# Performance work log

Measured on AMD Instinct MI355X. Metric: run time of the kernel, lower is better.

Reference implementation:

```python
import jax, jax.numpy as jnp
import numpy as np

NUM_HOP = 3
VOCAB = 32000
D = 512          # embed_dim
MEM = 60         # memory_size (> story_size -> T_A slice branch)
BS = 64
STORY = 50
SENT = 32        # max_sent_size
QLEN = 16


def positional_encoding(J, d):
    # pe[i-1, k-1] = 1 - i/J - (k/d) * (1 - 2*i/J), i in 1..J, k in 1..d
    i = jnp.arange(1, J + 1, dtype=jnp.float32)[:, None]
    k = jnp.arange(1, d + 1, dtype=jnp.float32)[None, :]
    return 1.0 - i / J - (k / d) * (1.0 - 2.0 * i / J)


def setup_inputs() -> dict:
    key = jax.random.key(0)
    kA, kT, kC, kQ = jax.random.split(key, 4)
    # stacked embedding tables A[0..num_hop], each (VOCAB, D), N(0, 0.1)
    A = jax.random.normal(kA, (NUM_HOP + 1, VOCAB, D), dtype=jnp.float32) * 0.1
    T_A = jax.random.normal(kT, (1, MEM, D), dtype=jnp.float32) * 0.1
    context = jax.random.randint(kC, (BS, STORY, SENT), 0, VOCAB)
    query = jax.random.randint(kQ, (BS, QLEN), 0, VOCAB)
    return {"context": context, "query": query, "A": A, "T_A": T_A}


def reference(context, query, A, T_A):
    # padding_idx=0: row 0 of every table is zero
    A = A.at[:, 0, :].set(0.0)
    pe = positional_encoding(SENT, D)              # (SENT, D)

    # query encoding: u = B(query).sum(axis=1), B = A[0]; dropout is identity at eval
    u = A[0][query].sum(axis=1)                    # (BS, D)

    for h in range(NUM_HOP):
        # memory embedding with positional encoding, summed over words
        m = (A[h][context] * pe).sum(axis=2)       # (BS, STORY, D)
        # temporal encoding: memory_size > story_size branch
        m = m + T_A[:, :STORY, :]
        # output embedding (no positional encoding applied in original)
        c = A[h + 1][context].sum(axis=2)          # (BS, STORY, D)
        p = jax.nn.softmax(jnp.einsum('bsd,bd->bs', m, u), axis=1)
        u = u + jnp.einsum('bs,bsd->bd', p, c)

    # W = A[-1].weight.T -> logits = u @ W
    logits = u @ A[NUM_HOP].T                      # (BS, VOCAB)
    return jax.nn.softmax(logits, axis=-1)
```

## Files before the change

kernel.cpp:

```cpp
#include <hip/hip_runtime.h>
#include <math.h>

#define NUM_HOP 3
#define VOCAB   32000
#define DIM     512
#define MEM     60
#define BS      64
#define STORY   50
#define SENT    32
#define QLEN    16

#define SZ      ((size_t)BS * STORY * DIM)
#define TBL     ((size_t)VOCAB * DIM)

typedef short v8s __attribute__((ext_vector_type(8)));
typedef float v4f __attribute__((ext_vector_type(4)));

static __device__ __forceinline__ ushort f2bf(float x) {
    union { float f; unsigned u; } v; v.f = x;
    unsigned r = (v.u + 0x7FFFu + ((v.u >> 16) & 1u)) >> 16;
    return (ushort)r;
}

__global__ __launch_bounds__(128) void k_gather(const float* __restrict__ A,
                                                const int*   __restrict__ ctx,
                                                const int*   __restrict__ query,
                                                float*       __restrict__ mw,
                                                float*       __restrict__ c,
                                                float*       __restrict__ u) {
    const unsigned blk = blockIdx.x;
    const int d = threadIdx.x * 4;
    if (blk >= 4u * BS * STORY) {
        const int b = blk - 4u * BS * STORY;
        const int* q = query + b * QLEN;
        float4 acc = make_float4(0.f, 0.f, 0.f, 0.f);
        for (int t = 0; t < QLEN; ++t) {
            const int idx = q[t];
            if (idx != 0) {
                const float4 a = *(const float4*)(A + (size_t)idx * DIM + d);
                acc.x += a.x; acc.y += a.y; acc.z += a.z; acc.w += a.w;
            }
        }
        *(float4*)(u + (size_t)b * DIM + d) = acc;
        return;
    }
    const unsigned pass = blk / (BS * STORY);
    const unsigned bs   = blk - pass * (BS * STORY);
    const float* table = A + (size_t)pass * TBL;
    const int*   cw    = ctx + bs * SENT;

    float4 m  = make_float4(0.f, 0.f, 0.f, 0.f);
    float4 cc = make_float4(0.f, 0.f, 0.f, 0.f);
    const float invD = 1.0f / (float)DIM;
    #pragma unroll 8
    for (int w = 0; w < SENT; ++w) {
        const int idx = cw[w];
        if (idx == 0) continue;
        const float4 a = *(const float4*)(table + (size_t)idx * DIM + d);
        const float aw = 1.0f - (float)(w + 1) * (1.0f / (float)SENT);
        const float bw = 1.0f - (float)(2 * (w + 1)) * (1.0f / (float)SENT);
        m.x = fmaf(a.x, aw - bw * (float)(d + 1) * invD, m.x);
        m.y = fmaf(a.y, aw - bw * (float)(d + 2) * invD, m.y);
        m.z = fmaf(a.z, aw - bw * (float)(d + 3) * invD, m.z);
        m.w = fmaf(a.w, aw - bw * (float)(d + 4) * invD, m.w);
        cc.x += a.x; cc.y += a.y; cc.z += a.z; cc.w += a.w;
    }
    if (pass < 3) *(float4*)(mw + (size_t)pass * SZ + (size_t)bs * DIM + d) = m;
    if (pass > 0) *(float4*)(c + (size_t)(pass - 1) * SZ + (size_t)bs * DIM + d) = cc;
}

__global__ __launch_bounds__(512) void k_hops(const float* __restrict__ mw,
                                              const float* __restrict__ c,
                                              const float* __restrict__ T_A,
                                              const float* __restrict__ u_g,
                                              ushort*      __restrict__ ubf) {
    const int b    = blockIdx.x;
    const int tid  = threadIdx.x;
    const int wave = tid >> 6;
    const int lane = tid & 63;
    __shared__ float su[DIM];
    __shared__ float sw[64];
    __shared__ float up[8][DIM];

    su[tid] = u_g[(size_t)b * DIM + tid];
    __syncthreads();

    for (int h = 0; h < NUM_HOP; ++h) {
        const float* mwh = mw + (size_t)h * SZ + (size_t)b * STORY * DIM;
        const float* ch  = c  + (size_t)h * SZ + (size_t)b * STORY * DIM;

        const float4 u0 = *(const float4*)(&su[lane * 8]);
        const float4 u1 = *(const float4*)(&su[lane * 8 + 4]);
        for (int s = wave; s < STORY; s += 8) {
            const float* mrow = mwh + (size_t)s * DIM + lane * 8;
            const float* trow = T_A + (size_t)s * DIM + lane * 8;
            const float4 m0 = *(const float4*)(mrow);
            const float4 m1 = *(const float4*)(mrow + 4);
            const float4 t0 = *(const float4*)(trow);
            const float4 t1 = *(const float4*)(trow + 4);
            float p = (m0.x + t0.x) * u0.x + (m0.y + t0.y) * u0.y +
                      (m0.z + t0.z) * u0.z + (m0.w + t0.w) * u0.w +
                      (m1.x + t1.x) * u1.x + (m1.y + t1.y) * u1.y +
                      (m1.z + t1.z) * u1.z + (m1.w + t1.w) * u1.w;
            for (int off = 32; off; off >>= 1) p += __shfl_down(p, off);
            if (lane == 0) sw[s] = p;
        }
        __syncthreads();

        if (tid < 64) {
            const float v = (tid < STORY) ? sw[tid] : -1e30f;
            float mx = v;
            for (int off = 32; off; off >>= 1) mx = fmaxf(mx, __shfl_down(mx, off));
            mx = __shfl(mx, 0);
            const float e = (tid < STORY) ? __expf(v - mx) : 0.f;
            float sm = e;
            for (int off = 32; off; off >>= 1) sm += __shfl_down(sm, off);
            sm = __shfl(sm, 0);
            if (tid < STORY) sw[tid] = e / sm;
        }
        __syncthreads();

        float4 a0 = make_float4(0.f, 0.f, 0.f, 0.f);
        float4 a1 = make_float4(0.f, 0.f, 0.f, 0.f);
        for (int s = wave; s < STORY; s += 8) {
            const float  w    = sw[s];
            const float* crow = ch + (size_t)s * DIM + lane * 8;
            const float4 c0 = *(const float4*)(crow);
            const float4 c1 = *(const float4*)(crow + 4);
            a0.x = fmaf(w, c0.x, a0.x); a0.y = fmaf(w, c0.y, a0.y);
            a0.z = fmaf(w, c0.z, a0.z); a0.w = fmaf(w, c0.w, a0.w);
            a1.x = fmaf(w, c1.x, a1.x); a1.y = fmaf(w, c1.y, a1.y);
            a1.z = fmaf(w, c1.z, a1.z); a1.w = fmaf(w, c1.w, a1.w);
        }
        *(float4*)(&up[wave][lane * 8])     = a0;
        *(float4*)(&up[wave][lane * 8 + 4]) = a1;
        __syncthreads();

        float add = 0.f;
        #pragma unroll
        for (int w = 0; w < 8; ++w) add += up[w][tid];
        su[tid] += add;
        __syncthreads();
    }

    ubf[(size_t)b * DIM + tid] = f2bf(su[tid]);
}

__global__ __launch_bounds__(256) void k_logits(const float*  __restrict__ A3,
                                                const ushort* __restrict__ ubf,
                                                float*        __restrict__ out) {
    __shared__ ushort Abf[64 * 128];
    __shared__ ushort Ubf[64 * 128];
    const int tid  = threadIdx.x;
    const int lane = tid & 63;
    const int wave = tid >> 6;
    const int i16  = lane & 15;
    const int quad = lane >> 4;
    const int row0 = blockIdx.x * 64;

    v4f acc[4];
    #pragma unroll
    for (int nt = 0; nt < 4; ++nt) acc[nt] = (v4f){0.f, 0.f, 0.f, 0.f};

    for (int ko = 0; ko < 4; ++ko) {
        __syncthreads();
        #pragma unroll
        for (int it = 0; it < 4; ++it) {
            const int i = it * 256 + tid;
            const int r = i >> 4, g = i & 15;
            const float* src = A3 + ((size_t)(row0 + r)) * DIM + ko * 128 + g * 8;
            const float4 f0 = *(const float4*)(src);
            const float4 f1 = *(const float4*)(src + 4);
            union { ushort h[8]; uint4 q; } pk;
            pk.h[0] = f2bf(f0.x); pk.h[1] = f2bf(f0.y);
            pk.h[2] = f2bf(f0.z); pk.h[3] = f2bf(f0.w);
            pk.h[4] = f2bf(f1.x); pk.h[5] = f2bf(f1.y);
            pk.h[6] = f2bf(f1.z); pk.h[7] = f2bf(f1.w);
            *(uint4*)(&Abf[r * 128 + ((g ^ (r & 7)) * 8)]) = pk.q;
        }
        #pragma unroll
        for (int it = 0; it < 4; ++it) {
            const int i = it * 256 + tid;
            const int n = i >> 4, g = i & 15;
            const uint4 v = *(const uint4*)(ubf + (size_t)n * DIM + ko * 128 + g * 8);
            *(uint4*)(&Ubf[n * 128 + ((g ^ (n & 7)) * 8)]) = v;
        }
        __syncthreads();

        const int arow = wave * 16 + i16;
        #pragma unroll
        for (int ki = 0; ki < 4; ++ki) {
            const int ga = ki * 4 + quad;
            const v8s a = *(const v8s*)(&Abf[arow * 128 + ((ga ^ (arow & 7)) * 8)]);
            #pragma unroll
            for (int nt = 0; nt < 4; ++nt) {
                const int n = nt * 16 + i16;
                const v8s bb = *(const v8s*)(&Ubf[n * 128 + ((ga ^ (n & 7)) * 8)]);
                acc[nt] = __builtin_amdgcn_mfma_f32_16x16x32_bf16(a, bb, acc[nt], 0, 0, 0);
            }
        }
    }

    const int vbase = row0 + wave * 16 + quad * 4;
    #pragma unroll
    for (int nt = 0; nt < 4; ++nt) {
        const int bcol = nt * 16 + i16;
        #pragma unroll
        for (int r = 0; r < 4; ++r)
            out[(size_t)bcol * VOCAB + vbase + r] = acc[nt][r];
    }
}

__global__ __launch_bounds__(1024) void k_vsm(float* __restrict__ out) {
    const int b   = blockIdx.x;
    const int tid = threadIdx.x;
    float* row = out + (size_t)b * VOCAB;
    __shared__ float red[16];
    __shared__ float bc;

    float x[32];
    #pragma unroll
    for (int k = 0; k < 31; ++k) x[k] = row[tid + k * 1024];
    const bool extra = (tid < VOCAB - 31 * 1024);
    x[31] = extra ? row[tid + 31 * 1024] : -1e30f;

    float mx = -1e30f;
    #pragma unroll
    for (int k = 0; k < 32; ++k) mx = fmaxf(mx, x[k]);
    for (int off = 32; off; off >>= 1) mx = fmaxf(mx, __shfl_down(mx, off));
    if ((tid & 63) == 0) red[tid >> 6] = mx;
    __syncthreads();
    if (tid < 64) {
        float v = (tid < 16) ? red[tid] : -1e30f;
        for (int off = 8; off; off >>= 1) v = fmaxf(v, __shfl_down(v, off));
        if (tid == 0) bc = v;
    }
    __syncthreads();
    mx = bc;
    __syncthreads();

    float sum = 0.f;
    #pragma unroll
    for (int k = 0; k < 32; ++k) { x[k] = __expf(x[k] - mx); sum += x[k]; }
    if (!extra) sum -= x[31];
    for (int off = 32; off; off >>= 1) sum += __shfl_down(sum, off);
    if ((tid & 63) == 0) red[tid >> 6] = sum;
    __syncthreads();
    if (tid < 64) {
        float v = (tid < 16) ? red[tid] : 0.f;
        for (int off = 8; off; off >>= 1) v += __shfl_down(v, off);
        if (tid == 0) bc = v;
    }
    __syncthreads();
    const float inv = 1.0f / bc;

    #pragma unroll
    for (int k = 0; k < 31; ++k) row[tid + k * 1024] = x[k] * inv;
    if (extra) row[tid + 31 * 1024] = x[31] * inv;
}

extern "C" void kernel_launch(void* const* d_in, const int* in_sizes, int n_in,
                              void* d_out, int out_size, void* d_ws, size_t ws_size,
                              hipStream_t stream) {
    const int*   ctx   = (const int*)d_in[0];
    const int*   query = (const int*)d_in[1];
    const float* A     = (const float*)d_in[2];
    const float* T_A   = (const float*)d_in[3];
    float* out = (float*)d_out;

    float*  u   = (float*)d_ws;
    ushort* ubf = (ushort*)(u + (size_t)BS * DIM);
    float*  mw  = (float*)(ubf + (size_t)BS * DIM);
    float*  c   = mw + 3 * SZ;

    k_gather<<<4 * BS * STORY + BS, 128, 0, stream>>>(A, ctx, query, mw, c, u);
    k_hops  <<<BS, 512, 0, stream>>>(mw, c, T_A, u, ubf);
    k_logits<<<VOCAB / 64, 256, 0, stream>>>(A + 3 * TBL, ubf, out);
    k_vsm   <<<BS, 1024, 0, stream>>>(out);
}
```

Baseline: 457.1 us.

## Replace memory gather with per-hop vocab projection and score gathering

```diff
diff --git a/kernel.cpp b/kernel.cpp
--- a/kernel.cpp
+++ b/kernel.cpp
@@ -10,157 +10,52 @@
 #define SENT    32
 #define QLEN    16
 
-#define SZ      ((size_t)BS * STORY * DIM)
 #define TBL     ((size_t)VOCAB * DIM)
 
-typedef short v8s __attribute__((ext_vector_type(8)));
-typedef float v4f __attribute__((ext_vector_type(4)));
-
-static __device__ __forceinline__ ushort f2bf(float x) {
-    union { float f; unsigned u; } v; v.f = x;
-    unsigned r = (v.u + 0x7FFFu + ((v.u >> 16) & 1u)) >> 16;
-    return (ushort)r;
-}
-
-__global__ __launch_bounds__(128) void k_gather(const float* __restrict__ A,
-                                                const int*   __restrict__ ctx,
-                                                const int*   __restrict__ query,
-                                                float*       __restrict__ mw,
-                                                float*       __restrict__ c,
-                                                float*       __restrict__ u) {
-    const unsigned blk = blockIdx.x;
-    const int d = threadIdx.x * 4;
-    if (blk >= 4u * BS * STORY) {
-        const int b = blk - 4u * BS * STORY;
-        const int* q = query + b * QLEN;
-        float4 acc = make_float4(0.f, 0.f, 0.f, 0.f);
-        for (int t = 0; t < QLEN; ++t) {
-            const int idx = q[t];
-            if (idx != 0) {
-                const float4 a = *(const float4*)(A + (size_t)idx * DIM + d);
-                acc.x += a.x; acc.y += a.y; acc.z += a.z; acc.w += a.w;
-            }
-        }
-        *(float4*)(u + (size_t)b * DIM + d) = acc;
-        return;
-    }
-    const unsigned pass = blk / (BS * STORY);
-    const unsigned bs   = blk - pass * (BS * STORY);
-    const float* table = A + (size_t)pass * TBL;
-    const int*   cw    = ctx + bs * SENT;
-
-    float4 m  = make_float4(0.f, 0.f, 0.f, 0.f);
-    float4 cc = make_float4(0.f, 0.f, 0.f, 0.f);
-    const float invD = 1.0f / (float)DIM;
-    #pragma unroll 8
-    for (int w = 0; w < SENT; ++w) {
-        const int idx = cw[w];
-        if (idx == 0) continue;
-        const float4 a = *(const float4*)(table + (size_t)idx * DIM + d);
-        const float aw = 1.0f - (float)(w + 1) * (1.0f / (float)SENT);
-        const float bw = 1.0f - (float)(2 * (w + 1)) * (1.0f / (float)SENT);
-        m.x = fmaf(a.x, aw - bw * (float)(d + 1) * invD, m.x);
-        m.y = fmaf(a.y, aw - bw * (float)(d + 2) * invD, m.y);
-        m.z = fmaf(a.z, aw - bw * (float)(d + 3) * invD, m.z);
-        m.w = fmaf(a.w, aw - bw * (float)(d + 4) * invD, m.w);
-        cc.x += a.x; cc.y += a.y; cc.z += a.z; cc.w += a.w;
-    }
-    if (pass < 3) *(float4*)(mw + (size_t)pass * SZ + (size_t)bs * DIM + d) = m;
-    if (pass > 0) *(float4*)(c + (size_t)(pass - 1) * SZ + (size_t)bs * DIM + d) = cc;
-}
-
-__global__ __launch_bounds__(512) void k_hops(const float* __restrict__ mw,
-                                              const float* __restrict__ c,
-                                              const float* __restrict__ T_A,
-                                              const float* __restrict__ u_g,
-                                              ushort*      __restrict__ ubf) {
-    const int b    = blockIdx.x;
-    const int tid  = threadIdx.x;
-    const int wave = tid >> 6;
-    const int lane = tid & 63;
-    __shared__ float su[DIM];
-    __shared__ float sw[64];
-    __shared__ float up[8][DIM];
-
-    su[tid] = u_g[(size_t)b * DIM + tid];
-    __syncthreads();
-
-    for (int h = 0; h < NUM_HOP; ++h) {
-        const float* mwh = mw + (size_t)h * SZ + (size_t)b * STORY * DIM;
-        const float* ch  = c  + (size_t)h * SZ + (size_t)b * STORY * DIM;
-
-        const float4 u0 = *(const float4*)(&su[lane * 8]);
-        const float4 u1 = *(const float4*)(&su[lane * 8 + 4]);
-        for (int s = wave; s < STORY; s += 8) {
-            const float* mrow = mwh + (size_t)s * DIM + lane * 8;
-            const float* trow = T_A + (size_t)s * DIM + lane * 8;
-            const float4 m0 = *(const float4*)(mrow);
-            const float4 m1 = *(const float4*)(mrow + 4);
-            const float4 t0 = *(const float4*)(trow);
-            const float4 t1 = *(const float4*)(trow + 4);
-            float p = (m0.x + t0.x) * u0.x + (m0.y + t0.y) * u0.y +
-                      (m0.z + t0.z) * u0.z + (m0.w + t0.w) * u0.w +
-                      (m1.x + t1.x) * u1.x + (m1.y + t1.y) * u1.y +
-                      (m1.z + t1.z) * u1.z + (m1.w + t1.w) * u1.w;
-            for (int off = 32; off; off >>= 1) p += __shfl_down(p, off);
-            if (lane == 0) sw[s] = p;
-        }
-        __syncthreads();
-
-        if (tid < 64) {
-            const float v = (tid < STORY) ? sw[tid] : -1e30f;
-            float mx = v;
-            for (int off = 32; off; off >>= 1) mx = fmaxf(mx, __shfl_down(mx, off));
-            mx = __shfl(mx, 0);
-            const float e = (tid < STORY) ? __expf(v - mx) : 0.f;
-            float sm = e;
-            for (int off = 32; off; off >>= 1) sm += __shfl_down(sm, off);
-            sm = __shfl(sm, 0);
-            if (tid < STORY) sw[tid] = e / sm;
-        }
-        __syncthreads();
-
-        float4 a0 = make_float4(0.f, 0.f, 0.f, 0.f);
-        float4 a1 = make_float4(0.f, 0.f, 0.f, 0.f);
-        for (int s = wave; s < STORY; s += 8) {
-            const float  w    = sw[s];
-            const float* crow = ch + (size_t)s * DIM + lane * 8;
-            const float4 c0 = *(const float4*)(crow);
-            const float4 c1 = *(const float4*)(crow + 4);
-            a0.x = fmaf(w, c0.x, a0.x); a0.y = fmaf(w, c0.y, a0.y);
-            a0.z = fmaf(w, c0.z, a0.z); a0.w = fmaf(w, c0.w, a0.w);
-            a1.x = fmaf(w, c1.x, a1.x); a1.y = fmaf(w, c1.y, a1.y);
-            a1.z = fmaf(w, c1.z, a1.z); a1.w = fmaf(w, c1.w, a1.w);
-        }
-        *(float4*)(&up[wave][lane * 8])     = a0;
-        *(float4*)(&up[wave][lane * 8 + 4]) = a1;
-        __syncthreads();
-
-        float add = 0.f;
-        #pragma unroll
-        for (int w = 0; w < 8; ++w) add += up[w][tid];
-        su[tid] += add;
-        __syncthreads();
-    }
-
-    ubf[(size_t)b * DIM + tid] = f2bf(su[tid]);
-}
-
-__global__ __launch_bounds__(256) void k_logits(const float*  __restrict__ A3,
-                                                const ushort* __restrict__ ubf,
-                                                float*        __restrict__ out) {
-    __shared__ ushort Abf[64 * 128];
-    __shared__ ushort Ubf[64 * 128];
+typedef _Float16 v8h __attribute__((ext_vector_type(8)));
+typedef float    v4f __attribute__((ext_vector_type(4)));
+
+static __device__ __forceinline__ ushort f2h(float x) {
+    union { _Float16 h; ushort u; } v;
+    v.h = (_Float16)x;
+    return v.u;
+}
+
+__global__ __launch_bounds__(512) void k_prep(const float* __restrict__ A0,
+                                              const int*   __restrict__ query,
+                                              float*       __restrict__ u,
+                                              ushort*      __restrict__ U2h) {
+    const int b = blockIdx.x, tid = threadIdx.x;
+    const int* q = query + b * QLEN;
+    int idx[QLEN];
+    #pragma unroll
+    for (int t = 0; t < QLEN; ++t) idx[t] = q[t];
+    float acc = 0.f;
+    #pragma unroll
+    for (int t = 0; t < QLEN; ++t)
+        if (idx[t] != 0) acc += A0[(size_t)idx[t] * DIM + tid];
+    u[(size_t)b * DIM + tid] = acc;
+    U2h[(size_t)b * DIM + tid] = f2h(acc);
+    U2h[(size_t)(BS + b) * DIM + tid] = f2h(acc * (float)(tid + 1) * (1.0f / (float)DIM));
+}
+
+__global__ __launch_bounds__(256) void k_z(const float*  __restrict__ Ah,
+                                           const float*  __restrict__ T_A,
+                                           const ushort* __restrict__ U2h,
+                                           float2*       __restrict__ Z2) {
+    __shared__ ushort Ah16[64 * 128];
+    __shared__ ushort Uh16[128 * 128];
     const int tid  = threadIdx.x;
     const int lane = tid & 63;
     const int wave = tid >> 6;
     const int i16  = lane & 15;
     const int quad = lane >> 4;
+    const bool ist = (blockIdx.x == 500);
     const int row0 = blockIdx.x * 64;
 
-    v4f acc[4];
-    #pragma unroll
-    for (int nt = 0; nt < 4; ++nt) acc[nt] = (v4f){0.f, 0.f, 0.f, 0.f};
+    v4f acc[8];
+    #pragma unroll
+    for (int nt = 0; nt < 8; ++nt) acc[nt] = (v4f){0.f, 0.f, 0.f, 0.f};
 
     for (int ko = 0; ko < 4; ++ko) {
         __syncthreads();
@@ -168,22 +63,23 @@
         for (int it = 0; it < 4; ++it) {
             const int i = it * 256 + tid;
             const int r = i >> 4, g = i & 15;
-            const float* src = A3 + ((size_t)(row0 + r)) * DIM + ko * 128 + g * 8;
+            const int rsrc = ist ? (r < MEM ? r : MEM - 1) : (row0 + r);
+            const float* src = (ist ? T_A : Ah) + (size_t)rsrc * DIM + ko * 128 + g * 8;
             const float4 f0 = *(const float4*)(src);
             const float4 f1 = *(const float4*)(src + 4);
             union { ushort h[8]; uint4 q; } pk;
-            pk.h[0] = f2bf(f0.x); pk.h[1] = f2bf(f0.y);
-            pk.h[2] = f2bf(f0.z); pk.h[3] = f2bf(f0.w);
-            pk.h[4] = f2bf(f1.x); pk.h[5] = f2bf(f1.y);
-            pk.h[6] = f2bf(f1.z); pk.h[7] = f2bf(f1.w);
-            *(uint4*)(&Abf[r * 128 + ((g ^ (r & 7)) * 8)]) = pk.q;
-        }
-        #pragma unroll
-        for (int it = 0; it < 4; ++it) {
+            pk.h[0] = f2h(f0.x); pk.h[1] = f2h(f0.y);
+            pk.h[2] = f2h(f0.z); pk.h[3] = f2h(f0.w);
+            pk.h[4] = f2h(f1.x); pk.h[5] = f2h(f1.y);
+            pk.h[6] = f2h(f1.z); pk.h[7] = f2h(f1.w);
+            *(uint4*)(&Ah16[r * 128 + ((g ^ (r & 7)) * 8)]) = pk.q;
+        }
+        #pragma unroll
+        for (int it = 0; it < 8; ++it) {
             const int i = it * 256 + tid;
             const int n = i >> 4, g = i & 15;
-            const uint4 v = *(const uint4*)(ubf + (size_t)n * DIM + ko * 128 + g * 8);
-            *(uint4*)(&Ubf[n * 128 + ((g ^ (n & 7)) * 8)]) = v;
+            const uint4 v = *(const uint4*)(U2h + (size_t)n * DIM + ko * 128 + g * 8);
+            *(uint4*)(&Uh16[n * 128 + ((g ^ (n & 7)) * 8)]) = v;
         }
         __syncthreads();
 
@@ -191,12 +87,12 @@
         #pragma unroll
         for (int ki = 0; ki < 4; ++ki) {
             const int ga = ki * 4 + quad;
-            const v8s a = *(const v8s*)(&Abf[arow * 128 + ((ga ^ (arow & 7)) * 8)]);
+            const v8h a = *(const v8h*)(&Ah16[arow * 128 + ((ga ^ (arow & 7)) * 8)]);
             #pragma unroll
-            for (int nt = 0; nt < 4; ++nt) {
+            for (int nt = 0; nt < 8; ++nt) {
                 const int n = nt * 16 + i16;
-                const v8s bb = *(const v8s*)(&Ubf[n * 128 + ((ga ^ (n & 7)) * 8)]);
-                acc[nt] = __builtin_amdgcn_mfma_f32_16x16x32_bf16(a, bb, acc[nt], 0, 0, 0);
+                const v8h bb = *(const v8h*)(&Uh16[n * 128 + ((ga ^ (n & 7)) * 8)]);
+                acc[nt] = __builtin_amdgcn_mfma_f32_16x16x32_f16(a, bb, acc[nt], 0, 0, 0);
             }
         }
     }
@@ -204,11 +100,151 @@
     const int vbase = row0 + wave * 16 + quad * 4;
     #pragma unroll
     for (int nt = 0; nt < 4; ++nt) {
-        const int bcol = nt * 16 + i16;
+        const int b = nt * 16 + i16;
         #pragma unroll
         for (int r = 0; r < 4; ++r)
-            out[(size_t)bcol * VOCAB + vbase + r] = acc[nt][r];
-    }
+            Z2[(size_t)(vbase + r) * BS + b] = make_float2(acc[nt][r], acc[nt + 4][r]);
+    }
+}
+
+__global__ __launch_bounds__(256) void k_score(const int*    __restrict__ ctx,
+                                               const float2* __restrict__ Z2,
+                                               float*        __restrict__ p) {
+    const int b    = blockIdx.x;
+    const int tid  = threadIdx.x;
+    const int wave = tid >> 6;
+    const int lane = tid & 63;
+    const int w    = lane & 31;
+    const int half = lane >> 5;
+    __shared__ float ss[64];
+
+    const float aw = 1.0f - (float)(w + 1) * (1.0f / 32.0f);
+    const float bw = 1.0f - (float)(w + 1) * (1.0f / 16.0f);
+
+    #pragma unroll
+    for (int i = 0; i < 7; ++i) {
+        const int s = i * 8 + wave * 2 + half;
+        float val = 0.f;
+        if (s < STORY) {
+            const int idx = ctx[b * (STORY * SENT) + s * SENT + w];
+            if (idx != 0) {
+                const float2 z = Z2[(size_t)idx * BS + b];
+                val = aw * z.x - bw * z.y;
+            }
+        }
+        val += __shfl_down(val, 16); val += __shfl_down(val, 8);
+        val += __shfl_down(val, 4);  val += __shfl_down(val, 2);
+        val += __shfl_down(val, 1);
+        if (w == 0 && s < STORY)
+            ss[s] = val + Z2[(size_t)(VOCAB + s) * BS + b].x;
+    }
+    __syncthreads();
+
+    if (tid < 64) {
+        const float v = (tid < STORY) ? ss[tid] : -1e30f;
+        float mx = v;
+        for (int off = 32; off; off >>= 1) mx = fmaxf(mx, __shfl_down(mx, off));
+        mx = __shfl(mx, 0);
+        const float e = (tid < STORY) ? __expf(v - mx) : 0.f;
+        float sm = e;
+        for (int off = 32; off; off >>= 1) sm += __shfl_down(sm, off);
+        sm = __shfl(sm, 0);
+        p[b * 64 + tid] = e / sm;
+    }
+}
+
+__global__ __launch_bounds__(256) void k_cupd(const int*   __restrict__ ctx,
+                                              const float* __restrict__ p,
+                                              const float* __restrict__ An,
+                                              float*       __restrict__ u,
+                                              ushort*      __restrict__ U2h) {
+    const int b    = blockIdx.x >> 3;
+    const int dc   = blockIdx.x & 7;
+    const int tid  = threadIdx.x;
+    const int wave = tid >> 6;
+    const int lane = tid & 63;
+    const int d    = dc * 64 + lane;
+    __shared__ float part[4][64];
+
+    const int*   cb = ctx + b * (STORY * SENT);
+    const float* pb = p + b * 64;
+
+    float acc = 0.f;
+    for (int t0 = wave * 400; t0 < wave * 400 + 400; t0 += 8) {
+        int idx[8]; float ps[8], av[8];
+        #pragma unroll
+        for (int j = 0; j < 8; ++j) idx[j] = cb[t0 + j];
+        #pragma unroll
+        for (int j = 0; j < 8; ++j) av[j] = An[(size_t)idx[j] * DIM + d];
+        #pragma unroll
+        for (int j = 0; j < 8; ++j) ps[j] = (idx[j] != 0) ? pb[(t0 + j) >> 5] : 0.f;
+        #pragma unroll
+        for (int j = 0; j < 8; ++j) acc = fmaf(av[j], ps[j], acc);
+    }
+    part[wave][lane] = acc;
+    __syncthreads();
+
+    if (tid < 64) {
+        const int dd = dc * 64 + tid;
+        const float un = u[(size_t)b * DIM + dd]
+                       + part[0][tid] + part[1][tid] + part[2][tid] + part[3][tid];
+        u[(size_t)b * DIM + dd] = un;
+        U2h[(size_t)b * DIM + dd] = f2h(un);
+        U2h[(size_t)(BS + b) * DIM + dd] = f2h(un * (float)(dd + 1) * (1.0f / (float)DIM));
+    }
+}
+
+#define DCH 64
+__global__ __launch_bounds__(256) void k_logits(const float* __restrict__ A3,
+                                                const float* __restrict__ u,
+                                                float*       __restrict__ out) {
+    __shared__ float AT[DCH][64];
+    __shared__ float UT[DCH][64];
+    const int tid = threadIdx.x;
+    const int v0  = blockIdx.x * 64;
+    const int vq  = (tid & 15) * 4;
+    const int bq  = (tid >> 4) * 4;
+    const int lr  = tid & 63;
+    const int dg  = tid >> 6;
+
+    float4 acc[4];
+    #pragma unroll
+    for (int j = 0; j < 4; ++j) acc[j] = make_float4(0.f, 0.f, 0.f, 0.f);
+
+    for (int ko = 0; ko < 8; ++ko) {
+        __syncthreads();
+        #pragma unroll
+        for (int k4 = 0; k4 < 4; ++k4) {
+            const int dd = dg * 16 + k4 * 4;
+            const float4 a = *(const float4*)(A3 + (size_t)(v0 + lr) * DIM + ko * DCH + dd);
+            AT[dd + 0][lr] = a.x; AT[dd + 1][lr] = a.y;
+            AT[dd + 2][lr] = a.z; AT[dd + 3][lr] = a.w;
+            const float4 b = *(const float4*)(u + (size_t)lr * DIM + ko * DCH + dd);
+            UT[dd + 0][lr] = b.x; UT[dd + 1][lr] = b.y;
+            UT[dd + 2][lr] = b.z; UT[dd + 3][lr] = b.w;
+        }
+        __syncthreads();
+        #pragma unroll 4
+        for (int dd = 0; dd < DCH; ++dd) {
+            const float4 a4 = *(const float4*)(&AT[dd][vq]);
+            const float4 u4 = *(const float4*)(&UT[dd][bq]);
+            acc[0].x = fmaf(a4.x, u4.x, acc[0].x); acc[0].y = fmaf(a4.y, u4.x, acc[0].y);
+            acc[0].z = fmaf(a4.z, u4.x, acc[0].z); acc[0].w = fmaf(a4.w, u4.x, acc[0].w);
+            acc[1].x = fmaf(a4.x, u4.y, acc[1].x); acc[1].y = fmaf(a4.y, u4.y, acc[1].y);
+            acc[1].z = fmaf(a4.z, u4.y, acc[1].z); acc[1].w = fmaf(a4.w, u4.y, acc[1].w);
+            acc[2].x = fmaf(a4.x, u4.z, acc[2].x); acc[2].y = fmaf(a4.y, u4.z, acc[2].y);
+            acc[2].z = fmaf(a4.z, u4.z, acc[2].z); acc[2].w = fmaf(a4.w, u4.z, acc[2].w);
+            acc[3].x = fmaf(a4.x, u4.w, acc[3].x); acc[3].y = fmaf(a4.y, u4.w, acc[3].y);
+            acc[3].z = fmaf(a4.z, u4.w, acc[3].z); acc[3].w = fmaf(a4.w, u4.w, acc[3].w);
+        }
+    }
+
+    if (v0 + vq == 0) {
+        acc[0].x = 0.f; acc[1].x = 0.f; acc[2].x = 0.f; acc[3].x = 0.f;
+    }
+    #pragma unroll
+    for (int j = 0; j < 4; ++j)
+        *(float4*)(out + (size_t)(bq + j) * VOCAB + v0 + vq) = acc[j];
 }
 
 __global__ __launch_bounds__(1024) void k_vsm(float* __restrict__ out) {
@@ -269,12 +305,16 @@
     float* out = (float*)d_out;
 
     float*  u   = (float*)d_ws;
-    ushort* ubf = (ushort*)(u + (size_t)BS * DIM);
-    float*  mw  = (float*)(ubf + (size_t)BS * DIM);
-    float*  c   = mw + 3 * SZ;
-
-    k_gather<<<4 * BS * STORY + BS, 128, 0, stream>>>(A, ctx, query, mw, c, u);
-    k_hops  <<<BS, 512, 0, stream>>>(mw, c, T_A, u, ubf);
-    k_logits<<<VOCAB / 64, 256, 0, stream>>>(A + 3 * TBL, ubf, out);
-    k_vsm   <<<BS, 1024, 0, stream>>>(out);
-}
+    ushort* U2h = (ushort*)(u + BS * DIM);
+    float*  p   = (float*)(U2h + 2 * BS * DIM);
+    float2* Z2  = (float2*)(p + BS * 64);
+
+    k_prep<<<BS, DIM, 0, stream>>>(A, query, u, U2h);
+    for (int h = 0; h < NUM_HOP; ++h) {
+        k_z    <<<501, 256, 0, stream>>>(A + (size_t)h * TBL, T_A, U2h, Z2);
+        k_score<<<BS, 256, 0, stream>>>(ctx, Z2, p);
+        k_cupd <<<BS * 8, 256, 0, stream>>>(ctx, p, A + (size_t)(h + 1) * TBL, u, U2h);
+    }
+    k_logits<<<500, 256, 0, stream>>>(A + 3 * TBL, u, out);
+    k_vsm  <<<BS, 1024, 0, stream>>>(out);
+}
```

Result: slower. 630.1 us (+37.9%).
